# Performance work log

Measured on AMD Instinct MI355X. Metric: run time of the kernel, lower is better.

## Reference

```python
import jax, jax.numpy as jnp
import numpy as np

N = 100000          # number of active sparse points
GRID = 800          # coordinate grid extent (2D)
KS = 9              # 3x3 kernel offsets
C_IN = 24
C_HID = 144         # round(24 * 6)
C_OUT = 24
EPS = 1e-5


def _build_kernel_map():
    """Build MinkowskiEngine-style kernel map for a 3x3 stride-1 channelwise conv.
    Returns (in_idx, out_idx, off_id), each [KS*N] int32. Invalid (no neighbor)
    entries point to sentinel row N so the padded gather/scatter is a no-op."""
    rng = np.random.default_rng(0)
    flat = rng.choice(GRID * GRID, size=N, replace=False)  # unique 2D coords
    ys, xs = flat // GRID, flat % GRID
    coord_to_idx = -np.ones(GRID * GRID, dtype=np.int64)
    coord_to_idx[flat] = np.arange(N)
    in_chunks, out_chunks, off_chunks = [], [], []
    pts = np.arange(N, dtype=np.int64)
    k = 0
    for dy in (-1, 0, 1):
        for dx in (-1, 0, 1):
            ny, nx = ys + dy, xs + dx
            inside = (ny >= 0) & (ny < GRID) & (nx >= 0) & (nx < GRID)
            nflat = np.clip(ny, 0, GRID - 1) * GRID + np.clip(nx, 0, GRID - 1)
            nidx = np.where(inside, coord_to_idx[nflat], -1)
            valid = nidx >= 0
            in_chunks.append(np.where(valid, nidx, N))
            out_chunks.append(np.where(valid, pts, N))
            off_chunks.append(np.full(N, k, dtype=np.int64))
            k += 1
    in_idx = np.concatenate(in_chunks).astype(np.int32)
    out_idx = np.concatenate(out_chunks).astype(np.int32)
    off_id = np.concatenate(off_chunks).astype(np.int32)
    return in_idx, out_idx, off_id


def setup_inputs() -> dict:
    key = jax.random.key(0)
    ks = jax.random.split(key, 4)
    in_idx, out_idx, off_id = _build_kernel_map()
    return {
        "feats": jax.random.normal(ks[0], (N, C_IN), jnp.float32),
        "w1": jax.random.normal(ks[1], (C_IN, C_HID), jnp.float32) * 0.1,
        "g1": jnp.ones((C_HID,), jnp.float32),
        "b1": jnp.zeros((C_HID,), jnp.float32),
        "w2": jax.random.normal(ks[2], (KS, C_HID), jnp.float32) * 0.1,
        "g2": jnp.ones((C_HID,), jnp.float32),
        "b2": jnp.zeros((C_HID,), jnp.float32),
        "w3": jax.random.normal(ks[3], (C_HID, C_OUT), jnp.float32) * 0.1,
        "g3": jnp.ones((C_OUT,), jnp.float32),
        "b3": jnp.zeros((C_OUT,), jnp.float32),
        "in_idx": jnp.asarray(in_idx),
        "out_idx": jnp.asarray(out_idx),
        "off_id": jnp.asarray(off_id),
    }


def _bn(x, g, b):
    # MinkowskiBatchNorm forward (training mode): per-channel stats over points
    m = jnp.mean(x, axis=0)
    v = jnp.var(x, axis=0)
    return (x - m) * jax.lax.rsqrt(v + EPS) * g + b


def _relu6(x):
    return jnp.clip(x, 0.0, 6.0)


def _channelwise_conv3x3(x, w2, in_idx, out_idx, off_id):
    # gather-multiply-scatter: out[p, c] = sum_k w2[k, c] * x[nbr_k(p), c]
    xp = jnp.concatenate([x, jnp.zeros((1, x.shape[1]), x.dtype)], axis=0)  # sentinel row
    contrib = xp[in_idx] * w2[off_id]                     # [KS*N, C_HID]
    out = jnp.zeros((N + 1, x.shape[1]), x.dtype).at[out_idx].add(contrib)
    return out[:N]


def reference(feats, w1, g1, b1, w2, g2, b2, w3, g3, b3, in_idx, out_idx, off_id):
    x = _relu6(_bn(feats @ w1, g1, b1))                   # 1x1 expand
    x = _relu6(_bn(_channelwise_conv3x3(x, w2, in_idx, out_idx, off_id), g2, b2))
    x = _bn(x @ w3, g3, b3)                               # 1x1 project
    return x + feats                                      # residual (in==out, stride==1)
```

## Files before the change

kernel.cpp:

```cpp
#include <hip/hip_runtime.h>
#include <hip/hip_fp16.h>

#define N_PTS 100000
#define KSZ 9
#define C_IN 24
#define C_HID 144
#define C_OUT 24
#define EPSV 1e-5f

#define X1N_B 0ull
#define X2_B  28800512ull
#define ST_B  57600512ull
#define Y3_B  0ull

#define MU1_F  0
#define M1_F   32
#define SUM2_F 640
#define SQ2_F  800
#define SUM3_F 960
#define SQ3_F  992
#define ST_FLOATS 1024

typedef float f4v __attribute__((ext_vector_type(4)));

__device__ inline float4 f4z() { return make_float4(0.f, 0.f, 0.f, 0.f); }
__device__ inline float4 f4_fma_s(float s, float4 b, float4 c) {
    return make_float4(fmaf(s, b.x, c.x), fmaf(s, b.y, c.y),
                       fmaf(s, b.z, c.z), fmaf(s, b.w, c.w));
}
__device__ inline float clamp6(float x) { return fminf(fmaxf(x, 0.f), 6.f); }

__global__ void k_init(char* wsb) {
    int t = threadIdx.x;
    float* STF = (float*)(wsb + ST_B);
    for (int i = t; i < ST_FLOATS; i += 256) STF[i] = 0.f;
    float* sent = (float*)(wsb + X1N_B + (size_t)N_PTS * (C_HID * 2));
    if (t < 72) sent[t] = 0.f;
}

__global__ void k_moments(const float* __restrict__ feats, char* __restrict__ wsb) {
    int t = threadIdx.x;
    float* STF = (float*)(wsb + ST_B);
    int len = (N_PTS + gridDim.x - 1) / gridDim.x;
    int r0 = blockIdx.x * len;
    int r1 = min(r0 + len, N_PTS);
    if (t >= 600) return;
    float a = 0.f;
    if (t < 576) {
        int i = t / 24, j = t % 24;
#pragma unroll 4
        for (int r = r0; r < r1; r++)
            a = fmaf(feats[(size_t)r * 24 + i], feats[(size_t)r * 24 + j], a);
        atomicAdd(&STF[M1_F + t], a);
    } else {
        int k = t - 576;
#pragma unroll 4
        for (int r = r0; r < r1; r++) a += feats[(size_t)r * 24 + k];
        atomicAdd(&STF[MU1_F + k], a);
    }
}

__global__ void __launch_bounds__(576, 5)
k_gemm1(const float* __restrict__ feats, const float* __restrict__ w1,
        const float* __restrict__ g1, const float* __restrict__ b1,
        char* __restrict__ wsb) {
    __shared__ float scs[C_HID], shs[C_HID];
    float* STF = (float*)(wsb + ST_B);
    int t = threadIdx.x;
    if (t < C_HID) {
        float wc[C_IN];
#pragma unroll
        for (int k = 0; k < C_IN; k++) wc[k] = w1[k * C_HID + t];
        const float invN = 1.f / (float)N_PTS;
        float mean = 0.f;
#pragma unroll
        for (int k = 0; k < C_IN; k++) mean = fmaf(STF[MU1_F + k], wc[k], mean);
        mean *= invN;
        float e2 = 0.f;
        for (int i = 0; i < C_IN; i++) {
            float s = 0.f;
#pragma unroll
            for (int j = 0; j < C_IN; j++) s = fmaf(STF[M1_F + i * 24 + j], wc[j], s);
            e2 = fmaf(wc[i], s, e2);
        }
        e2 *= invN;
        float var = e2 - mean * mean;
        float s1 = g1[t] * rsqrtf(var + EPSV);
        scs[t] = s1;
        shs[t] = b1[t] - mean * s1;
    }
    __syncthreads();
    int c = t % C_HID, pg = t / C_HID;
    float sc = scs[c];
    float sh = shs[c];
    float wreg[C_IN];
#pragma unroll
    for (int k = 0; k < C_IN; k++) wreg[k] = w1[k * C_HID + c] * sc;
    __half* x1h = (__half*)(wsb + X1N_B);
    for (int p = blockIdx.x * 4 + pg; p < N_PTS; p += gridDim.x * 4) {
        const float4* fr = (const float4*)(feats + (size_t)p * C_IN);
        float acc = sh;
#pragma unroll
        for (int q = 0; q < 6; q++) {
            float4 f = fr[q];
            acc = fmaf(f.x, wreg[4 * q + 0], acc);
            acc = fmaf(f.y, wreg[4 * q + 1], acc);
            acc = fmaf(f.z, wreg[4 * q + 2], acc);
            acc = fmaf(f.w, wreg[4 * q + 3], acc);
        }
        x1h[(size_t)p * C_HID + c] = __float2half_rn(clamp6(acc));
    }
}

__global__ void k_conv(const float* __restrict__ w2, const int* __restrict__ in_idx,
                       char* __restrict__ wsb) {
    __shared__ float w2s[KSZ * C_HID];
    __shared__ float lsum[C_HID], lsq[C_HID];
    float* STF = (float*)(wsb + ST_B);
    int t = threadIdx.x;
    for (int e = t; e < KSZ * C_HID; e += 256) w2s[e] = w2[e];
    if (t < C_HID) { lsum[t] = 0.f; lsq[t] = 0.f; }
    __syncthreads();
    const __half* x1h = (const __half*)(wsb + X1N_B);
    __half* x2h = (__half*)(wsb + X2_B);
    const bool act = t < 252;
    int pt = t / 18, g = t % 18, c0 = g * 8;
    float rs[8], rq[8];
#pragma unroll
    for (int j = 0; j < 8; j++) { rs[j] = 0.f; rq[j] = 0.f; }
    const int nChunks = (N_PTS + 13) / 14;
    int ch = (int)blockIdx.x;
    int p = ch * 14 + pt;
    bool ok = act && p < N_PTS;
    int idxs[KSZ];
#pragma unroll
    for (int k = 0; k < KSZ; k++) idxs[k] = ok ? in_idx[k * N_PTS + p] : N_PTS;
    while (ch < nChunks) {
        float4 vv[KSZ];
#pragma unroll
        for (int k = 0; k < KSZ; k++)
            vv[k] = *(const float4*)(x1h + (size_t)idxs[k] * C_HID + c0);
        int chn = ch + (int)gridDim.x;
        int pn = chn * 14 + pt;
        bool okn = act && chn < nChunks && pn < N_PTS;
        int idxn[KSZ];
#pragma unroll
        for (int k = 0; k < KSZ; k++) idxn[k] = okn ? in_idx[k * N_PTS + pn] : N_PTS;
        float acc[8];
#pragma unroll
        for (int j = 0; j < 8; j++) acc[j] = 0.f;
#pragma unroll
        for (int k = 0; k < KSZ; k++) {
            union { float4 f; __half2 h[4]; } u;
            u.f = vv[k];
#pragma unroll
            for (int jj = 0; jj < 4; jj++) {
                float2 x = __half22float2(u.h[jj]);
                acc[2 * jj]     = fmaf(w2s[k * C_HID + c0 + 2 * jj],     x.x, acc[2 * jj]);
                acc[2 * jj + 1] = fmaf(w2s[k * C_HID + c0 + 2 * jj + 1], x.y, acc[2 * jj + 1]);
            }
        }
        if (ok) {
            union { f4v f; __half2 h[4]; } o;
#pragma unroll
            for (int jj = 0; jj < 4; jj++)
                o.h[jj] = __float22half2_rn(make_float2(acc[2 * jj], acc[2 * jj + 1]));
            __builtin_nontemporal_store(o.f, (f4v*)(x2h + (size_t)p * C_HID + c0));
#pragma unroll
            for (int j = 0; j < 8; j++) {
                rs[j] += acc[j];
                rq[j] = fmaf(acc[j], acc[j], rq[j]);
            }
        }
        ch = chn; p = pn; ok = okn;
#pragma unroll
        for (int k = 0; k < KSZ; k++) idxs[k] = idxn[k];
    }
    if (act) {
#pragma unroll
        for (int j = 0; j < 8; j++) {
            atomicAdd(&lsum[c0 + j], rs[j]);
            atomicAdd(&lsq[c0 + j], rq[j]);
        }
    }
    __syncthreads();
    if (t < C_HID) {
        atomicAdd(&STF[SUM2_F + t], lsum[t]);
        atomicAdd(&STF[SQ2_F + t], lsq[t]);
    }
}

__global__ void k_gemm2(const float* __restrict__ w3, const float* __restrict__ g2,
                        const float* __restrict__ b2, char* __restrict__ wsb) {
    __shared__ float4 w3s[C_HID * 6];
    __shared__ float4 sc2v[C_HID / 4], sh2v[C_HID / 4];
    float* STF = (float*)(wsb + ST_B);
    int t = threadIdx.x;
    for (int e = t; e < C_HID * 6; e += 256) w3s[e] = ((const float4*)w3)[e];
    if (t < C_HID) {
        const float invN = 1.f / (float)N_PTS;
        float mean = STF[SUM2_F + t] * invN;
        float var = STF[SQ2_F + t] * invN - mean * mean;
        float s = g2[t] * rsqrtf(var + EPSV);
        ((float*)sc2v)[t] = s;
        ((float*)sh2v)[t] = b2[t] - mean * s;
    }
    __syncthreads();
    int r = blockIdx.x * 256 + t;
    if (r >= N_PTS) return;
    const float4* x2v = (const float4*)(wsb + X2_B + (size_t)r * (C_HID * 2));
    float4 a[6];
#pragma unroll
    for (int c4 = 0; c4 < 6; c4++) a[c4] = f4z();
#pragma unroll 6
    for (int h8 = 0; h8 < 18; h8++) {
        union { float4 f; __half2 h[4]; } u;
        u.f = x2v[h8];
        float4 s0 = sc2v[2 * h8], s1 = sc2v[2 * h8 + 1];
        float4 b0 = sh2v[2 * h8], b1 = sh2v[2 * h8 + 1];
        float2 x0 = __half22float2(u.h[0]);
        float2 x1 = __half22float2(u.h[1]);
        float2 x2 = __half22float2(u.h[2]);
        float2 x3 = __half22float2(u.h[3]);
        float xs[8];
        xs[0] = clamp6(fmaf(x0.x, s0.x, b0.x));
        xs[1] = clamp6(fmaf(x0.y, s0.y, b0.y));
        xs[2] = clamp6(fmaf(x1.x, s0.z, b0.z));
        xs[3] = clamp6(fmaf(x1.y, s0.w, b0.w));
        xs[4] = clamp6(fmaf(x2.x, s1.x, b1.x));
        xs[5] = clamp6(fmaf(x2.y, s1.y, b1.y));
        xs[6] = clamp6(fmaf(x3.x, s1.z, b1.z));
        xs[7] = clamp6(fmaf(x3.y, s1.w, b1.w));
#pragma unroll
        for (int j = 0; j < 8; j++) {
            int h = h8 * 8 + j;
#pragma unroll
            for (int c4 = 0; c4 < 6; c4++)
                a[c4] = f4_fma_s(xs[j], w3s[h * 6 + c4], a[c4]);
        }
    }
    float4* y3v = (float4*)(wsb + Y3_B) + (size_t)r * 6;
#pragma unroll
    for (int c4 = 0; c4 < 6; c4++) y3v[c4] = a[c4];
}

__global__ void k_red3(char* __restrict__ wsb) {
    int t = threadIdx.x;
    const float* y3 = (const float*)(wsb + Y3_B);
    float* STF = (float*)(wsb + ST_B);
    float rs = 0.f, rq = 0.f;
    const int total = N_PTS * C_OUT;
    for (int e = blockIdx.x * 192 + t; e < total; e += gridDim.x * 192) {
        float v = y3[e];
        rs += v;
        rq = fmaf(v, v, rq);
    }
    __shared__ float ls[192], lq[192];
    ls[t] = rs; lq[t] = rq;
    __syncthreads();
    if (t < C_OUT) {
        float s = 0.f, q = 0.f;
        for (int u = t; u < 192; u += C_OUT) { s += ls[u]; q += lq[u]; }
        atomicAdd(&STF[SUM3_F + t], s);
        atomicAdd(&STF[SQ3_F + t], q);
    }
}

__global__ void k_out(const float* __restrict__ feats, const float* __restrict__ g3,
                      const float* __restrict__ b3, const char* __restrict__ wsb,
                      float* __restrict__ out) {
    __shared__ float s3[C_OUT], h3[C_OUT];
    const float* STF = (const float*)(wsb + ST_B);
    int t = threadIdx.x;
    if (t < C_OUT) {
        const float invN = 1.f / (float)N_PTS;
        float mean = STF[SUM3_F + t] * invN;
        float var = STF[SQ3_F + t] * invN - mean * mean;
        float s = g3[t] * rsqrtf(var + EPSV);
        s3[t] = s;
        h3[t] = b3[t] - mean * s;
    }
    __syncthreads();
    int tau = blockIdx.x * 256 + t;
    if (tau >= N_PTS * 6) return;
    int c = (tau % 6) * 4;
    float4 y = ((const float4*)(wsb + Y3_B))[tau];
    float4 f = ((const float4*)feats)[tau];
    float4 o;
    o.x = fmaf(y.x, s3[c + 0], h3[c + 0]) + f.x;
    o.y = fmaf(y.y, s3[c + 1], h3[c + 1]) + f.y;
    o.z = fmaf(y.z, s3[c + 2], h3[c + 2]) + f.z;
    o.w = fmaf(y.w, s3[c + 3], h3[c + 3]) + f.w;
    ((float4*)out)[tau] = o;
}

extern "C" void kernel_launch(void* const* d_in, const int* in_sizes, int n_in,
                              void* d_out, int out_size, void* d_ws, size_t ws_size,
                              hipStream_t stream) {
    const float* feats = (const float*)d_in[0];
    const float* w1 = (const float*)d_in[1];
    const float* g1 = (const float*)d_in[2];
    const float* b1 = (const float*)d_in[3];
    const float* w2 = (const float*)d_in[4];
    const float* g2 = (const float*)d_in[5];
    const float* b2 = (const float*)d_in[6];
    const float* w3 = (const float*)d_in[7];
    const float* g3 = (const float*)d_in[8];
    const float* b3 = (const float*)d_in[9];
    const int* in_idx = (const int*)d_in[10];
    char* wsb = (char*)d_ws;
    float* out = (float*)d_out;

    hipLaunchKernelGGL(k_init, dim3(1), dim3(256), 0, stream, wsb);
    hipLaunchKernelGGL(k_moments, dim3(256), dim3(640), 0, stream, feats, wsb);
    hipLaunchKernelGGL(k_gemm1, dim3(1024), dim3(576), 0, stream, feats, w1, g1, b1, wsb);
    hipLaunchKernelGGL(k_conv, dim3(2048), dim3(256), 0, stream, w2, in_idx, wsb);
    hipLaunchKernelGGL(k_gemm2, dim3((N_PTS + 255) / 256), dim3(256), 0, stream, w3, g2, b2, wsb);
    hipLaunchKernelGGL(k_red3, dim3(512), dim3(192), 0, stream, wsb);
    hipLaunchKernelGGL(k_out, dim3((N_PTS * 6 + 255) / 256), dim3(256), 0, stream,
                       feats, g3, b3, wsb, out);
}
```

Measured before the change: 292.6 us.

## Restructure conv gather with double-buffered narrower lanes and fuse BN3 stats into gemm2

The depthwise conv kernel now gives each thread 4 channels instead of 8 and keeps the weights in registers instead of shared memory. It processes 7 points per block chunk and double-buffers gathers across two chunks so loads overlap compute. The separate k_red3 reduction pass is folded into gemm2 through wave shuffles and a small shared reduction, which removes a full re-read of y3. The init kernel is replaced by hipMemsetAsync calls. Narrower 8-byte gathers may use memory bandwidth less efficiently, and the extra atomics per block add some contention.

```diff
diff --git a/kernel.cpp b/kernel.cpp
--- a/kernel.cpp
+++ b/kernel.cpp
@@ -7,6 +7,8 @@
 #define C_HID 144
 #define C_OUT 24
 #define EPSV 1e-5f
+#define CPTS 7
+#define NCH ((N_PTS + CPTS - 1) / CPTS)
 
 #define X1N_B 0ull
 #define X2_B  28800512ull
@@ -19,9 +21,8 @@
 #define SQ2_F  800
 #define SUM3_F 960
 #define SQ3_F  992
-#define ST_FLOATS 1024
-
-typedef float f4v __attribute__((ext_vector_type(4)));
+
+typedef float f2v __attribute__((ext_vector_type(2)));
 
 __device__ inline float4 f4z() { return make_float4(0.f, 0.f, 0.f, 0.f); }
 __device__ inline float4 f4_fma_s(float s, float4 b, float4 c) {
@@ -29,14 +30,6 @@
                        fmaf(s, b.z, c.z), fmaf(s, b.w, c.w));
 }
 __device__ inline float clamp6(float x) { return fminf(fmaxf(x, 0.f), 6.f); }
-
-__global__ void k_init(char* wsb) {
-    int t = threadIdx.x;
-    float* STF = (float*)(wsb + ST_B);
-    for (int i = t; i < ST_FLOATS; i += 256) STF[i] = 0.f;
-    float* sent = (float*)(wsb + X1N_B + (size_t)N_PTS * (C_HID * 2));
-    if (t < 72) sent[t] = 0.f;
-}
 
 __global__ void k_moments(const float* __restrict__ feats, char* __restrict__ wsb) {
     int t = threadIdx.x;
@@ -112,73 +105,78 @@
     }
 }
 
-__global__ void k_conv(const float* __restrict__ w2, const int* __restrict__ in_idx,
-                       char* __restrict__ wsb) {
-    __shared__ float w2s[KSZ * C_HID];
+__device__ inline void cissue(int ch, int pt, bool act, const int* __restrict__ in_idx,
+                              const __half* __restrict__ x1h, int c0, f2v vv[KSZ]) {
+    int p = ch * CPTS + pt;
+    bool ok = act && ch < NCH && p < N_PTS;
+    int pcl = ok ? p : 0;
+    int idxs[KSZ];
+#pragma unroll
+    for (int k = 0; k < KSZ; k++) idxs[k] = ok ? in_idx[k * N_PTS + pcl] : N_PTS;
+#pragma unroll
+    for (int k = 0; k < KSZ; k++)
+        vv[k] = *(const f2v*)(x1h + (size_t)idxs[k] * C_HID + c0);
+}
+
+__device__ inline void ccomp(int ch, int pt, bool act, const float4 wr[KSZ], int c0,
+                             __half* __restrict__ x2h, const f2v vv[KSZ],
+                             float rs[4], float rq[4]) {
+    int p = ch * CPTS + pt;
+    bool ok = act && p < N_PTS;
+    float a0 = 0.f, a1 = 0.f, a2 = 0.f, a3 = 0.f;
+#pragma unroll
+    for (int k = 0; k < KSZ; k++) {
+        union { f2v f; __half2 h[2]; } u;
+        u.f = vv[k];
+        float2 lo = __half22float2(u.h[0]);
+        float2 hi = __half22float2(u.h[1]);
+        a0 = fmaf(wr[k].x, lo.x, a0);
+        a1 = fmaf(wr[k].y, lo.y, a1);
+        a2 = fmaf(wr[k].z, hi.x, a2);
+        a3 = fmaf(wr[k].w, hi.y, a3);
+    }
+    if (ok) {
+        union { f2v f; __half2 h[2]; } o;
+        o.h[0] = __float22half2_rn(make_float2(a0, a1));
+        o.h[1] = __float22half2_rn(make_float2(a2, a3));
+        __builtin_nontemporal_store(o.f, (f2v*)(x2h + (size_t)p * C_HID + c0));
+    }
+    rs[0] += a0; rs[1] += a1; rs[2] += a2; rs[3] += a3;
+    rq[0] = fmaf(a0, a0, rq[0]); rq[1] = fmaf(a1, a1, rq[1]);
+    rq[2] = fmaf(a2, a2, rq[2]); rq[3] = fmaf(a3, a3, rq[3]);
+}
+
+__global__ void __launch_bounds__(256, 4)
+k_conv(const float* __restrict__ w2, const int* __restrict__ in_idx,
+       char* __restrict__ wsb) {
     __shared__ float lsum[C_HID], lsq[C_HID];
     float* STF = (float*)(wsb + ST_B);
     int t = threadIdx.x;
-    for (int e = t; e < KSZ * C_HID; e += 256) w2s[e] = w2[e];
     if (t < C_HID) { lsum[t] = 0.f; lsq[t] = 0.f; }
+    bool act = t < 252;
+    int pt = t / 36, g = t % 36, c0 = g * 4;
+    float4 wr[KSZ];
+#pragma unroll
+    for (int k = 0; k < KSZ; k++) wr[k] = *(const float4*)(w2 + k * C_HID + c0);
     __syncthreads();
     const __half* x1h = (const __half*)(wsb + X1N_B);
     __half* x2h = (__half*)(wsb + X2_B);
-    const bool act = t < 252;
-    int pt = t / 18, g = t % 18, c0 = g * 8;
-    float rs[8], rq[8];
-#pragma unroll
-    for (int j = 0; j < 8; j++) { rs[j] = 0.f; rq[j] = 0.f; }
-    const int nChunks = (N_PTS + 13) / 14;
-    int ch = (int)blockIdx.x;
-    int p = ch * 14 + pt;
-    bool ok = act && p < N_PTS;
-    int idxs[KSZ];
-#pragma unroll
-    for (int k = 0; k < KSZ; k++) idxs[k] = ok ? in_idx[k * N_PTS + p] : N_PTS;
-    while (ch < nChunks) {
-        float4 vv[KSZ];
-#pragma unroll
-        for (int k = 0; k < KSZ; k++)
-            vv[k] = *(const float4*)(x1h + (size_t)idxs[k] * C_HID + c0);
-        int chn = ch + (int)gridDim.x;
-        int pn = chn * 14 + pt;
-        bool okn = act && chn < nChunks && pn < N_PTS;
-        int idxn[KSZ];
-#pragma unroll
-        for (int k = 0; k < KSZ; k++) idxn[k] = okn ? in_idx[k * N_PTS + pn] : N_PTS;
-        float acc[8];
-#pragma unroll
-        for (int j = 0; j < 8; j++) acc[j] = 0.f;
-#pragma unroll
-        for (int k = 0; k < KSZ; k++) {
-            union { float4 f; __half2 h[4]; } u;
-            u.f = vv[k];
-#pragma unroll
-            for (int jj = 0; jj < 4; jj++) {
-                float2 x = __half22float2(u.h[jj]);
-                acc[2 * jj]     = fmaf(w2s[k * C_HID + c0 + 2 * jj],     x.x, acc[2 * jj]);
-                acc[2 * jj + 1] = fmaf(w2s[k * C_HID + c0 + 2 * jj + 1], x.y, acc[2 * jj + 1]);
-            }
-        }
-        if (ok) {
-            union { f4v f; __half2 h[4]; } o;
-#pragma unroll
-            for (int jj = 0; jj < 4; jj++)
-                o.h[jj] = __float22half2_rn(make_float2(acc[2 * jj], acc[2 * jj + 1]));
-            __builtin_nontemporal_store(o.f, (f4v*)(x2h + (size_t)p * C_HID + c0));
-#pragma unroll
-            for (int j = 0; j < 8; j++) {
-                rs[j] += acc[j];
-                rq[j] = fmaf(acc[j], acc[j], rq[j]);
-            }
-        }
-        ch = chn; p = pn; ok = okn;
-#pragma unroll
-        for (int k = 0; k < KSZ; k++) idxs[k] = idxn[k];
+    float rs[4] = {0.f, 0.f, 0.f, 0.f}, rq[4] = {0.f, 0.f, 0.f, 0.f};
+    f2v va[KSZ], vb[KSZ];
+    int chA = (int)blockIdx.x, chB = chA + (int)gridDim.x;
+    cissue(chA, pt, act, in_idx, x1h, c0, va);
+    while (chA < NCH) {
+        cissue(chB, pt, act, in_idx, x1h, c0, vb);
+        ccomp(chA, pt, act, wr, c0, x2h, va, rs, rq);
+        chA = chB + (int)gridDim.x;
+        if (chB >= NCH) break;
+        cissue(chA, pt, act, in_idx, x1h, c0, va);
+        ccomp(chB, pt, act, wr, c0, x2h, vb, rs, rq);
+        chB = chA + (int)gridDim.x;
     }
     if (act) {
 #pragma unroll
-        for (int j = 0; j < 8; j++) {
+        for (int j = 0; j < 4; j++) {
             atomicAdd(&lsum[c0 + j], rs[j]);
             atomicAdd(&lsq[c0 + j], rq[j]);
         }
@@ -194,6 +192,7 @@
                         const float* __restrict__ b2, char* __restrict__ wsb) {
     __shared__ float4 w3s[C_HID * 6];
     __shared__ float4 sc2v[C_HID / 4], sh2v[C_HID / 4];
+    __shared__ float red[192];
     float* STF = (float*)(wsb + ST_B);
     int t = threadIdx.x;
     for (int e = t; e < C_HID * 6; e += 256) w3s[e] = ((const float4*)w3)[e];
@@ -207,62 +206,68 @@
     }
     __syncthreads();
     int r = blockIdx.x * 256 + t;
-    if (r >= N_PTS) return;
-    const float4* x2v = (const float4*)(wsb + X2_B + (size_t)r * (C_HID * 2));
+    bool ok = r < N_PTS;
     float4 a[6];
 #pragma unroll
     for (int c4 = 0; c4 < 6; c4++) a[c4] = f4z();
-#pragma unroll 6
-    for (int h8 = 0; h8 < 18; h8++) {
-        union { float4 f; __half2 h[4]; } u;
-        u.f = x2v[h8];
-        float4 s0 = sc2v[2 * h8], s1 = sc2v[2 * h8 + 1];
-        float4 b0 = sh2v[2 * h8], b1 = sh2v[2 * h8 + 1];
-        float2 x0 = __half22float2(u.h[0]);
-        float2 x1 = __half22float2(u.h[1]);
-        float2 x2 = __half22float2(u.h[2]);
-        float2 x3 = __half22float2(u.h[3]);
-        float xs[8];
-        xs[0] = clamp6(fmaf(x0.x, s0.x, b0.x));
-        xs[1] = clamp6(fmaf(x0.y, s0.y, b0.y));
-        xs[2] = clamp6(fmaf(x1.x, s0.z, b0.z));
-        xs[3] = clamp6(fmaf(x1.y, s0.w, b0.w));
-        xs[4] = clamp6(fmaf(x2.x, s1.x, b1.x));
-        xs[5] = clamp6(fmaf(x2.y, s1.y, b1.y));
-        xs[6] = clamp6(fmaf(x3.x, s1.z, b1.z));
-        xs[7] = clamp6(fmaf(x3.y, s1.w, b1.w));
-#pragma unroll
-        for (int j = 0; j < 8; j++) {
-            int h = h8 * 8 + j;
-#pragma unroll
-            for (int c4 = 0; c4 < 6; c4++)
-                a[c4] = f4_fma_s(xs[j], w3s[h * 6 + c4], a[c4]);
-        }
-    }
-    float4* y3v = (float4*)(wsb + Y3_B) + (size_t)r * 6;
-#pragma unroll
-    for (int c4 = 0; c4 < 6; c4++) y3v[c4] = a[c4];
-}
-
-__global__ void k_red3(char* __restrict__ wsb) {
-    int t = threadIdx.x;
-    const float* y3 = (const float*)(wsb + Y3_B);
-    float* STF = (float*)(wsb + ST_B);
-    float rs = 0.f, rq = 0.f;
-    const int total = N_PTS * C_OUT;
-    for (int e = blockIdx.x * 192 + t; e < total; e += gridDim.x * 192) {
-        float v = y3[e];
-        rs += v;
-        rq = fmaf(v, v, rq);
-    }
-    __shared__ float ls[192], lq[192];
-    ls[t] = rs; lq[t] = rq;
-    __syncthreads();
-    if (t < C_OUT) {
-        float s = 0.f, q = 0.f;
-        for (int u = t; u < 192; u += C_OUT) { s += ls[u]; q += lq[u]; }
-        atomicAdd(&STF[SUM3_F + t], s);
-        atomicAdd(&STF[SQ3_F + t], q);
+    if (ok) {
+        const float4* x2v = (const float4*)(wsb + X2_B + (size_t)r * (C_HID * 2));
+#pragma unroll 3
+        for (int h8 = 0; h8 < 18; h8++) {
+            union { float4 f; __half2 h[4]; } u;
+            u.f = x2v[h8];
+            float4 s0 = sc2v[2 * h8], s1 = sc2v[2 * h8 + 1];
+            float4 b0 = sh2v[2 * h8], b1v = sh2v[2 * h8 + 1];
+            float2 x0 = __half22float2(u.h[0]);
+            float2 x1 = __half22float2(u.h[1]);
+            float2 x2 = __half22float2(u.h[2]);
+            float2 x3 = __half22float2(u.h[3]);
+            float xs[8];
+            xs[0] = clamp6(fmaf(x0.x, s0.x, b0.x));
+            xs[1] = clamp6(fmaf(x0.y, s0.y, b0.y));
+            xs[2] = clamp6(fmaf(x1.x, s0.z, b0.z));
+            xs[3] = clamp6(fmaf(x1.y, s0.w, b0.w));
+            xs[4] = clamp6(fmaf(x2.x, s1.x, b1v.x));
+            xs[5] = clamp6(fmaf(x2.y, s1.y, b1v.y));
+            xs[6] = clamp6(fmaf(x3.x, s1.z, b1v.z));
+            xs[7] = clamp6(fmaf(x3.y, s1.w, b1v.w));
+#pragma unroll
+            for (int j = 0; j < 8; j++) {
+                int h = h8 * 8 + j;
+#pragma unroll
+                for (int c4 = 0; c4 < 6; c4++)
+                    a[c4] = f4_fma_s(xs[j], w3s[h * 6 + c4], a[c4]);
+            }
+        }
+        float4* y3v = (float4*)(wsb + Y3_B) + (size_t)r * 6;
+#pragma unroll
+        for (int c4 = 0; c4 < 6; c4++) y3v[c4] = a[c4];
+    }
+    int wv = t >> 6, ln = t & 63;
+#pragma unroll
+    for (int c4 = 0; c4 < 6; c4++) {
+        float4 s = a[c4];
+        float4 q = make_float4(s.x * s.x, s.y * s.y, s.z * s.z, s.w * s.w);
+#pragma unroll
+        for (int m = 1; m < 64; m <<= 1) {
+            s.x += __shfl_xor(s.x, m); s.y += __shfl_xor(s.y, m);
+            s.z += __shfl_xor(s.z, m); s.w += __shfl_xor(s.w, m);
+            q.x += __shfl_xor(q.x, m); q.y += __shfl_xor(q.y, m);
+            q.z += __shfl_xor(q.z, m); q.w += __shfl_xor(q.w, m);
+        }
+        if (ln == 0) {
+            int base = wv * 48 + c4 * 4;
+            red[base + 0] = s.x; red[base + 1] = s.y;
+            red[base + 2] = s.z; red[base + 3] = s.w;
+            red[base + 24 + 0] = q.x; red[base + 24 + 1] = q.y;
+            red[base + 24 + 2] = q.z; red[base + 24 + 3] = q.w;
+        }
+    }
+    __syncthreads();
+    if (t < 48) {
+        float v = red[t] + red[48 + t] + red[96 + t] + red[144 + t];
+        if (t < 24) atomicAdd(&STF[SUM3_F + t], v);
+        else        atomicAdd(&STF[SQ3_F + t - 24], v);
     }
 }
 
@@ -311,12 +316,14 @@
     char* wsb = (char*)d_ws;
     float* out = (float*)d_out;
 
-    hipLaunchKernelGGL(k_init, dim3(1), dim3(256), 0, stream, wsb);
+    (void)hipMemsetAsync(wsb + ST_B, 0, 4096, stream);
+    (void)hipMemsetAsync(wsb + (size_t)N_PTS * C_HID * 2, 0, C_HID * 2, stream);
+
     hipLaunchKernelGGL(k_moments, dim3(256), dim3(640), 0, stream, feats, wsb);
     hipLaunchKernelGGL(k_gemm1, dim3(1024), dim3(576), 0, stream, feats, w1, g1, b1, wsb);
     hipLaunchKernelGGL(k_conv, dim3(2048), dim3(256), 0, stream, w2, in_idx, wsb);
-    hipLaunchKernelGGL(k_gemm2, dim3((N_PTS + 255) / 256), dim3(256), 0, stream, w3, g2, b2, wsb);
-    hipLaunchKernelGGL(k_red3, dim3(512), dim3(192), 0, stream, wsb);
+    hipLaunchKernelGGL(k_gemm2, dim3((N_PTS + 255) / 256), dim3(256), 0, stream,
+                       w3, g2, b2, wsb);
     hipLaunchKernelGGL(k_out, dim3((N_PTS * 6 + 255) / 256), dim3(256), 0, stream,
                        feats, g3, b3, wsb, out);
 }
```

Result: slower. 304.1 us (+3.9%).
